# Performance work log

Hardware: AMD Instinct MI355X
Metric: run time of the kernel (lower is better)

## Reference

```python
import jax, jax.numpy as jnp
import numpy as np

N5, N4, N3, K = 10242, 2562, 642, 7  # icosphere node counts (levels 5,4,3), spatial kernel size
M = 32  # mchannel
EPS = 1e-8


def _sconv(x, neigh, W, b, relu=True):
    # x: [B,T,N,Cin]; neigh: [N,K] 1-ring indices; W: [K,Cin,Cout]
    xn = x[:, :, neigh, :]                        # [B,T,N,K,Cin] irregular gather
    y = jnp.einsum('btnkc,kcd->btnd', xn, W) + b  # per-node kernel contraction
    return jax.nn.relu(y) if relu else y


def _spool(x, pidx):
    # max-pool fine->coarse mesh: pidx [Ncoarse,Kp] indexes fine nodes
    return jnp.max(x[:, :, pidx, :], axis=3)


def _unpool(x, uidx):
    # coarse->fine copy: uidx [Nfine] indexes coarse nodes
    return x[:, :, uidx, :]


def _cos(f, a):
    # torch.nn.CosineSimilarity(dim=-1): dot / max(|f|*|a|, eps)
    dot = jnp.sum(f * a, axis=-1)
    nf = jnp.linalg.norm(f, axis=-1)
    na = jnp.linalg.norm(a, axis=-1)
    return dot / jnp.maximum(nf * na, EPS)


def setup_inputs() -> dict:
    key = jax.random.key(0)
    ks = jax.random.split(key, 32)
    w = lambda i, shape: jax.random.normal(ks[i], shape, jnp.float32) * 0.05
    inp = {
        'frame': jax.random.normal(ks[0], (1, 16, N5, 3), jnp.float32),
        'aem': jax.random.normal(ks[1], (1, 16, N5), jnp.float32),
        'W0f': w(2, (K, 3, M)),        'b0f': w(3, (M,)),
        'W0a': w(4, (K, 1, M)),        'b0a': w(5, (M,)),
        'W1f': w(6, (K, M, 2 * M)),    'b1f': w(7, (2 * M,)),
        'W1a': w(8, (K, M, 2 * M)),    'b1a': w(9, (2 * M,)),
        'W2f': w(10, (K, 2 * M, 4 * M)), 'b2f': w(11, (4 * M,)),
        'W2a': w(12, (K, 2 * M, 4 * M)), 'b2a': w(13, (4 * M,)),
        'W7': w(14, (K, 12 * M, 2 * M)), 'b7': w(15, (2 * M,)),
        'W8': w(16, (K, 4 * M, M)),    'b8': w(17, (M,)),
        'W9': w(18, (K, M, 1)),        'b9': w(19, (1,)),
        'neigh5': jax.random.randint(ks[20], (N5, K), 0, N5),
        'neigh4': jax.random.randint(ks[21], (N4, K), 0, N4),
        'neigh3': jax.random.randint(ks[22], (N3, K), 0, N3),
        'pool5': jax.random.randint(ks[23], (N4, K), 0, N5),
        'pool4': jax.random.randint(ks[24], (N3, K), 0, N4),
        'up4': jax.random.randint(ks[25], (N4,), 0, N3),
        'up5': jax.random.randint(ks[26], (N5,), 0, N4),
        'Tlocation': jax.random.randint(ks[27], (1, 16), 0, 16),
    }
    return inp


def reference(frame, aem, W0f, b0f, W0a, b0a, W1f, b1f, W1a, b1a, W2f, b2f,
              W2a, b2a, W7, b7, W8, b8, W9, b9,
              neigh5, neigh4, neigh3, pool5, pool4, up4, up5, Tlocation):
    a = aem[..., None]                                    # [B,T,N5,1]
    # encoder level 0 (N5)
    c0f = _sconv(frame, neigh5, W0f, b0f)
    c0a = _sconv(a, neigh5, W0a, b0a)
    p0f = _spool(c0f, pool5)
    p0a = _spool(c0a, pool5)
    m0 = _cos(c0f, c0a)[..., None]                        # [B,T,N5,1]
    c0f_att, c0a_att = c0f * m0, c0a * m0
    # encoder level 1 (N4)
    c1f = _sconv(p0f, neigh4, W1f, b1f)
    c1a = _sconv(p0a, neigh4, W1a, b1a)
    p1f = _spool(c1f, pool4)
    p1a = _spool(c1a, pool4)
    m1 = _cos(c1f, c1a)[..., None]
    c1f_att, c1a_att = c1f * m1, c1a * m1
    # bottleneck (N3)
    c2f = _sconv(p1f, neigh3, W2f, b2f)
    c2a = _sconv(p1a, neigh3, W2a, b2a)
    m2 = _cos(c2f, c2a)[..., None]
    conv2 = jnp.concatenate((c2f * m2, c2a * m2), axis=-1)  # [B,T,N3,8M]
    # decoder
    cat7 = jnp.concatenate((_unpool(conv2, up4), c1f_att, c1a_att), axis=-1)  # [B,T,N4,12M]
    conv7 = _sconv(cat7, neigh4, W7, b7)
    cat8 = jnp.concatenate((_unpool(conv7, up5), c0f_att, c0a_att), axis=-1)  # [B,T,N5,4M]
    conv8 = _sconv(cat8, neigh5, W8, b8)
    conv9 = _sconv(conv8, neigh5, W9, b9, relu=False)[..., 0]  # [B,T,N5]
    return jax.nn.softmax(conv9, axis=-1)
```

## Files before the change

### kernel.cpp

```cpp
#include <hip/hip_runtime.h>
#include <cfloat>
#include <cstdint>


constexpr int T  = 16;
constexpr int n5 = 10242, n4 = 2562, n3 = 642;
constexpr int K  = 7;

using bf16x8 = __attribute__((ext_vector_type(8))) short;
using f32x4  = __attribute__((ext_vector_type(4))) float;

static __device__ __forceinline__ float bf2f(unsigned short u) {
    return __uint_as_float((unsigned)u << 16);
}
static __device__ __forceinline__ unsigned short f2bf(float x) {
    unsigned u = __float_as_uint(x);
    u += 0x7FFF + ((u >> 16) & 1);
    return (unsigned short)(u >> 16);
}

__global__ __launch_bounds__(256) void conv0_kernel(
    const float* __restrict__ frame, const float* __restrict__ aem,
    const float* __restrict__ W0f, const float* __restrict__ b0f,
    const float* __restrict__ W0a, const float* __restrict__ b0a,
    const int* __restrict__ neigh5,
    unsigned short* __restrict__ c0f, unsigned short* __restrict__ c0a,
    unsigned short* __restrict__ att0)
{
    const int g = threadIdx.x >> 5;
    const int d = threadIdx.x & 31;
    const int per_t = (n5 + 7) / 8;
    const int t = blockIdx.x / per_t;
    const int n = (blockIdx.x % per_t) * 8 + g;
    if (n >= n5) return;

    float accf = b0f[d];
    float acca = b0a[d];
    const int* nb = neigh5 + n * K;
    #pragma unroll
    for (int k = 0; k < K; ++k) {
        const int j = nb[k];
        const float* fr = frame + ((size_t)t * n5 + j) * 3;
        const float av = aem[(size_t)t * n5 + j];
        accf = fmaf(fr[0], W0f[(k * 3 + 0) * 32 + d], accf);
        accf = fmaf(fr[1], W0f[(k * 3 + 1) * 32 + d], accf);
        accf = fmaf(fr[2], W0f[(k * 3 + 2) * 32 + d], accf);
        acca = fmaf(av, W0a[k * 32 + d], acca);
    }
    accf = fmaxf(accf, 0.f);
    acca = fmaxf(acca, 0.f);

    float dot = accf * acca, ff = accf * accf, aa = acca * acca;
    #pragma unroll
    for (int m = 1; m < 32; m <<= 1) {
        dot += __shfl_xor(dot, m, 32);
        ff  += __shfl_xor(ff,  m, 32);
        aa  += __shfl_xor(aa,  m, 32);
    }
    const float mm = dot / fmaxf(sqrtf(ff) * sqrtf(aa), 1e-8f);
    const size_t base = ((size_t)t * n5 + n) * 32;
    c0f[base + d] = f2bf(accf);
    c0a[base + d] = f2bf(acca);
    const size_t abase = ((size_t)t * n5 + n) * 64;
    att0[abase + d]      = f2bf(accf * mm);
    att0[abase + 32 + d] = f2bf(acca * mm);
}

template<int C>
__global__ __launch_bounds__(256) void pool_kernel(
    const unsigned short* __restrict__ in, const int* __restrict__ pidx,
    int Nin, int Nout, unsigned short* __restrict__ out)
{
    constexpr int C8 = C / 8;
    const int idx = blockIdx.x * 256 + threadIdx.x;
    if (idx >= T * Nout * C8) return;
    const int c8 = idx % C8;
    const int n  = (idx / C8) % Nout;
    const int t  = idx / (C8 * Nout);
    const int* pp = pidx + n * K;
    float m[8];
    #pragma unroll
    for (int j = 0; j < 8; ++j) m[j] = -FLT_MAX;
    #pragma unroll
    for (int k = 0; k < K; ++k) {
        const uint4 v = reinterpret_cast<const uint4*>(in)[((size_t)t * Nin + pp[k]) * C8 + c8];
        const unsigned short* s = reinterpret_cast<const unsigned short*>(&v);
        #pragma unroll
        for (int j = 0; j < 8; ++j) m[j] = fmaxf(m[j], bf2f(s[j]));
    }
    unsigned short o[8];
    #pragma unroll
    for (int j = 0; j < 8; ++j) o[j] = f2bf(m[j]);
    reinterpret_cast<uint4*>(out)[((size_t)t * Nout + n) * C8 + c8] =
        *reinterpret_cast<const uint4*>(o);
}

template<int C, int NN>
__global__ __launch_bounds__(256) void cosatt_kernel(
    const unsigned short* __restrict__ f, const unsigned short* __restrict__ a,
    unsigned short* __restrict__ att)
{
    constexpr int CPL = C / 64;
    const int w = threadIdx.x >> 6, lane = threadIdx.x & 63;
    const int idx = blockIdx.x * 4 + w;
    if (idx >= T * NN) return;
    const unsigned short* fr = f + (size_t)idx * C;
    const unsigned short* ar = a + (size_t)idx * C;
    float xs[CPL], ys[CPL];
    float dot = 0.f, ff = 0.f, aa = 0.f;
    #pragma unroll
    for (int i = 0; i < CPL; ++i) {
        const float x = bf2f(fr[lane + i * 64]);
        const float y = bf2f(ar[lane + i * 64]);
        xs[i] = x; ys[i] = y;
        dot = fmaf(x, y, dot);
        ff  = fmaf(x, x, ff);
        aa  = fmaf(y, y, aa);
    }
    #pragma unroll
    for (int msk = 1; msk < 64; msk <<= 1) {
        dot += __shfl_xor(dot, msk);
        ff  += __shfl_xor(ff,  msk);
        aa  += __shfl_xor(aa,  msk);
    }
    const float m = dot / fmaxf(sqrtf(ff) * sqrtf(aa), 1e-8f);
    unsigned short* orow = att + (size_t)idx * 2 * C;
    #pragma unroll
    for (int i = 0; i < CPL; ++i) {
        orow[lane + i * 64]     = f2bf(xs[i] * m);
        orow[C + lane + i * 64] = f2bf(ys[i] * m);
    }
}

struct PlainB16 {
    const uint4* x; int N; int C8;
    struct Ref { int o; };
    __device__ __forceinline__ Ref prep(int t, int node) const {
        return { (int)(((size_t)t * N + node) * C8) };
    }
    __device__ __forceinline__ uint4 chunk(const Ref& r, int c8) const {
        return x[r.o + c8];
    }
};

struct Cat7B16 {
    const uint4* att2; const uint4* att1; const int* up4;
    struct Ref { int o2, o1; };
    __device__ __forceinline__ Ref prep(int t, int node) const {
        return { (int)(((size_t)t * n3 + up4[node]) * 32),
                 (int)(((size_t)t * n4 + node) * 16) };
    }
    __device__ __forceinline__ uint4 chunk(const Ref& r, int c8) const {
        return (c8 < 32) ? att2[r.o2 + c8] : att1[r.o1 + (c8 - 32)];
    }
};

struct Cat8B16 {
    const uint4* cv7; const uint4* att0; const int* up5;
    struct Ref { int o7, o0; };
    __device__ __forceinline__ Ref prep(int t, int node) const {
        return { (int)(((size_t)t * n4 + up5[node]) * 8),
                 (int)(((size_t)t * n5 + node) * 8) };
    }
    __device__ __forceinline__ uint4 chunk(const Ref& r, int c8) const {
        return (c8 < 8) ? cv7[r.o7 + c8] : att0[r.o0 + (c8 - 8)];
    }
};

__global__ __launch_bounds__(256) void wprep_all_kernel(
    const float* __restrict__ W1f, const float* __restrict__ W1a,
    const float* __restrict__ W2f, const float* __restrict__ W2a,
    const float* __restrict__ W7,  const float* __restrict__ W8,
    unsigned short* __restrict__ Wt1f, unsigned short* __restrict__ Wt1a,
    unsigned short* __restrict__ Wt2f, unsigned short* __restrict__ Wt2a,
    unsigned short* __restrict__ Wt7,  unsigned short* __restrict__ Wt8)
{
    int idx = blockIdx.x * 256 + threadIdx.x;
    const float* W; unsigned short* Wt; int KCv, CO;
    if (idx < 14336)       { W = W1f; Wt = Wt1f; KCv = 224;  CO = 64;  }
    else if (idx < 28672)  { idx -= 14336;  W = W1a; Wt = Wt1a; KCv = 224;  CO = 64;  }
    else if (idx < 86016)  { idx -= 28672;  W = W2f; Wt = Wt2f; KCv = 448;  CO = 128; }
    else if (idx < 143360) { idx -= 86016;  W = W2a; Wt = Wt2a; KCv = 448;  CO = 128; }
    else if (idx < 315392) { idx -= 143360; W = W7;  Wt = Wt7;  KCv = 2688; CO = 64;  }
    else                   { idx -= 315392; W = W8;  Wt = Wt8;  KCv = 896;  CO = 32;  }
    const int d = idx / KCv, kc = idx - d * KCv;
    Wt[idx] = f2bf(W[(size_t)kc * CO + d]);
}

template<int CIN, int COUT, int BM, class Loader>
__global__ __launch_bounds__(256) void gemm_kk_kernel(
    Loader ldr, int N, int Mt,
    const unsigned short* __restrict__ Wt,
    unsigned short* __restrict__ Z)
{
    constexpr int KC     = K * CIN;
    constexpr int BK     = 64;
    constexpr int KSTEPS = CIN / BK;
    constexpr int U4R    = BK / 8;
    constexpr int WGR_N  = COUT / 32;
    constexpr int WGR_M  = 4 / WGR_N;
    constexpr int VPTA   = BM * U4R / 256;
    static_assert(BM == WGR_M * 32 && CIN % BK == 0);

    __shared__ __align__(16) unsigned short As[KSTEPS][BM * BK];
    __shared__ __align__(16) unsigned short Cs[BM * COUT];

    const int xcd = blockIdx.x & 7;
    int idx = blockIdx.x >> 3;
    const int hi = (idx >= Mt) ? 1 : 0;
    const int t  = 2 * xcd + hi;
    const int tile_m = idx - hi * Mt;
    const int m0 = tile_m * BM;

    const int tid = threadIdx.x, lane = tid & 63, wave = tid >> 6;
    const int wr = wave / WGR_N, wc = wave % WGR_N;
    const int l15 = lane & 15, lhi = lane >> 4;

    typename Loader::Ref ref[VPTA];
    #pragma unroll
    for (int v = 0; v < VPTA; ++v) {
        const int row = (tid + v * 256) / U4R;
        ref[v] = ldr.prep(t, min(m0 + row, N - 1));
    }
    #pragma unroll
    for (int ks = 0; ks < KSTEPS; ++ks) {
        #pragma unroll
        for (int v = 0; v < VPTA; ++v) {
            const int g = tid + v * 256, row = g / U4R, c8 = g % U4R;
            const uint4 av = ldr.chunk(ref[v], ks * U4R + c8);
            *reinterpret_cast<uint4*>(&As[ks][(row * BK + c8 * 8) ^ ((row & 7) << 3)]) = av;
        }
    }

    const unsigned short* w0p = Wt + (size_t)(wc * 32 + l15) * KC + lhi * 8;
    const unsigned short* w1p = w0p + (size_t)16 * KC;

    __syncthreads();

    for (int kk = 0; kk < K; ++kk) {
        f32x4 acc[2][2] = {};
        #pragma unroll
        for (int ks = 0; ks < KSTEPS; ++ks) {
            #pragma unroll
            for (int kk2 = 0; kk2 < 2; ++kk2) {
                const int kb = kk2 * 32 + lhi * 8;
                bf16x8 a[2], b[2];
                #pragma unroll
                for (int m = 0; m < 2; ++m) {
                    const int row = wr * 32 + m * 16 + l15;
                    a[m] = *reinterpret_cast<const bf16x8*>(
                        &As[ks][(row * BK + kb) ^ ((row & 7) << 3)]);
                }
                const int woff = kk * CIN + ks * BK + kk2 * 32;
                b[0] = *reinterpret_cast<const bf16x8*>(w0p + woff);
                b[1] = *reinterpret_cast<const bf16x8*>(w1p + woff);
                #pragma unroll
                for (int m = 0; m < 2; ++m)
                    #pragma unroll
                    for (int n = 0; n < 2; ++n)
                        acc[m][n] = __builtin_amdgcn_mfma_f32_16x16x32_bf16(
                            a[m], b[n], acc[m][n], 0, 0, 0);
            }
        }

        __syncthreads();
        #pragma unroll
        for (int n = 0; n < 2; ++n) {
            const int col = wc * 32 + n * 16 + l15;
            #pragma unroll
            for (int m = 0; m < 2; ++m)
                #pragma unroll
                for (int i = 0; i < 4; ++i)
                    Cs[(wr * 32 + m * 16 + lhi * 4 + i) * COUT + col] = f2bf(acc[m][n][i]);
        }
        __syncthreads();
        constexpr int RPT = COUT / 8;
        constexpr int CV  = BM * COUT / 8 / 256;
        #pragma unroll
        for (int v = 0; v < CV; ++v) {
            const int g = tid + v * 256, row = g / RPT, c8 = g % RPT;
            const int grow = m0 + row;
            if (grow < N)
                *reinterpret_cast<uint4*>(
                    &Z[(((size_t)kk * T + t) * N + grow) * COUT + c8 * 8]) =
                    *reinterpret_cast<const uint4*>(&Cs[row * COUT + c8 * 8]);
        }
    }
}

template<int COUT>
__global__ __launch_bounds__(256) void epi_p_kernel(
    const unsigned short* __restrict__ Z, const int* __restrict__ neigh,
    int N, int Bt, const float* __restrict__ bias, unsigned short* __restrict__ out)
{
    constexpr int C8 = COUT / 8;
    const int xcd = blockIdx.x & 7;
    int idx = blockIdx.x >> 3;
    const int hi = (idx >= Bt) ? 1 : 0;
    const int t  = 2 * xcd + hi;
    const int e  = (idx - hi * Bt) * 256 + threadIdx.x;
    if (e >= N * C8) return;
    const int c8 = e % C8;
    const int n  = e / C8;
    const int* nb = neigh + n * K;

    float s[8];
    #pragma unroll
    for (int j = 0; j < 8; ++j) s[j] = bias[c8 * 8 + j];
    #pragma unroll
    for (int k = 0; k < K; ++k) {
        const uint4 v = *reinterpret_cast<const uint4*>(
            &Z[(((size_t)k * T + t) * N + nb[k]) * COUT + c8 * 8]);
        const unsigned short* p = reinterpret_cast<const unsigned short*>(&v);
        #pragma unroll
        for (int j = 0; j < 8; ++j) s[j] += bf2f(p[j]);
    }
    unsigned short o[8];
    #pragma unroll
    for (int j = 0; j < 8; ++j) o[j] = f2bf(fmaxf(s[j], 0.f));
    *reinterpret_cast<uint4*>(&out[((size_t)t * N + n) * COUT + c8 * 8]) =
        *reinterpret_cast<const uint4*>(o);
}

template<int CIN, int COUT, class Loader>
__device__ __forceinline__ void sconv_tile(
    const Loader& ldr, const int* __restrict__ neigh, int N, int t,
    int tile_m, int tile_n,
    const unsigned short* __restrict__ Wt, const float* __restrict__ bias,
    unsigned short* __restrict__ out)
{
    constexpr int KC     = K * CIN;
    constexpr int CHUNKS = CIN / 32;
    constexpr int STEPS  = K * CHUNKS;
    constexpr int D      = STEPS < 3 ? STEPS : 3;

    const int lane = threadIdx.x & 63;
    const int l15 = lane & 15, lhi = lane >> 4;

    const int r0 = tile_m * 32 + l15;
    const int row0 = min(r0, N - 1), row1 = min(r0 + 16, N - 1);

    typename Loader::Ref ref0[K], ref1[K];
    #pragma unroll
    for (int k = 0; k < K; ++k) {
        ref0[k] = ldr.prep(t, neigh[row0 * K + k]);
        ref1[k] = ldr.prep(t, neigh[row1 * K + k]);
    }

    const int col0 = tile_n * 32 + l15;
    const unsigned short* w0p = Wt + (size_t)col0 * KC + lhi * 8;
    const unsigned short* w1p = w0p + (size_t)16 * KC;

    uint4 qa0[D], qa1[D], qb0[D], qb1[D];

    auto issue = [&](int s, int slot) {
        const int k = s / CHUNKS, c = s - k * CHUNKS;
        const int c8 = c * 4 + lhi;
        qa0[slot] = ldr.chunk(ref0[k], c8);
        qa1[slot] = ldr.chunk(ref1[k], c8);
        qb0[slot] = *reinterpret_cast<const uint4*>(w0p + k * CIN + c * 32);
        qb1[slot] = *reinterpret_cast<const uint4*>(w1p + k * CIN + c * 32);
    };

    f32x4 acc[2][2] = {};

    #pragma unroll
    for (int s = 0; s < D; ++s) issue(s, s);
    __builtin_amdgcn_sched_barrier(0);

    #pragma unroll
    for (int s = 0; s < STEPS; ++s) {
        const int slot = s % D;
        const bf16x8 a0 = __builtin_bit_cast(bf16x8, qa0[slot]);
        const bf16x8 a1 = __builtin_bit_cast(bf16x8, qa1[slot]);
        const bf16x8 b0 = __builtin_bit_cast(bf16x8, qb0[slot]);
        const bf16x8 b1 = __builtin_bit_cast(bf16x8, qb1[slot]);
        acc[0][0] = __builtin_amdgcn_mfma_f32_16x16x32_bf16(a0, b0, acc[0][0], 0, 0, 0);
        acc[0][1] = __builtin_amdgcn_mfma_f32_16x16x32_bf16(a0, b1, acc[0][1], 0, 0, 0);
        acc[1][0] = __builtin_amdgcn_mfma_f32_16x16x32_bf16(a1, b0, acc[1][0], 0, 0, 0);
        acc[1][1] = __builtin_amdgcn_mfma_f32_16x16x32_bf16(a1, b1, acc[1][1], 0, 0, 0);
        if (s + D < STEPS) issue(s + D, slot);
        __builtin_amdgcn_sched_barrier(0);
    }

    #pragma unroll
    for (int n = 0; n < 2; ++n) {
        const int gcol = tile_n * 32 + n * 16 + l15;
        const float bv = bias[gcol];
        #pragma unroll
        for (int m = 0; m < 2; ++m) {
            #pragma unroll
            for (int i = 0; i < 4; ++i) {
                const int grow = tile_m * 32 + m * 16 + lhi * 4 + i;
                if (grow < N)
                    out[((size_t)t * N + grow) * COUT + gcol] =
                        f2bf(fmaxf(acc[m][n][i] + bv, 0.f));
            }
        }
    }
}

template<int CIN, int COUT, class Loader>
__global__ __launch_bounds__(64, 2) void sconv_rd2_kernel(
    Loader lf, Loader la, const int* __restrict__ neigh, int N, int U,
    const unsigned short* __restrict__ Wtf, const unsigned short* __restrict__ Wta,
    const float* __restrict__ bf_, const float* __restrict__ ba_,
    unsigned short* __restrict__ of_, unsigned short* __restrict__ oa_)
{
    constexpr int TN = COUT / 32;
    const int xcd = blockIdx.x & 7;
    int idx = blockIdx.x >> 3;
    const int sel = idx & 1; idx >>= 1;
    const int hi = (idx >= U) ? 1 : 0;
    const int t  = 2 * xcd + hi;
    const int w  = idx - hi * U;
    const Loader L = sel ? la : lf;
    const unsigned short* Wt = sel ? Wta : Wtf;
    const float* bias = sel ? ba_ : bf_;
    unsigned short* out = sel ? oa_ : of_;
    sconv_tile<CIN, COUT, Loader>(L, neigh, N, t, w / TN, w % TN, Wt, bias, out);
}

__global__ __launch_bounds__(256) void conv9_kernel(
    const unsigned short* __restrict__ cv8, const int* __restrict__ neigh5,
    const float* __restrict__ W9, const float* __restrict__ b9,
    float* __restrict__ logits)
{
    const int idx = blockIdx.x * 256 + threadIdx.x;
    if (idx >= T * n5) return;
    const int n = idx % n5;
    const int t = idx / n5;
    float acc = b9[0];
    const int* nb = neigh5 + n * K;
    #pragma unroll
    for (int k = 0; k < K; ++k) {
        const uint4* row = reinterpret_cast<const uint4*>(cv8 + ((size_t)t * n5 + nb[k]) * 32);
        const float* wk = W9 + k * 32;
        #pragma unroll
        for (int c4 = 0; c4 < 4; ++c4) {
            const uint4 v = row[c4];
            const unsigned short* s = reinterpret_cast<const unsigned short*>(&v);
            #pragma unroll
            for (int jj = 0; jj < 8; ++jj)
                acc = fmaf(bf2f(s[jj]), wk[c4 * 8 + jj], acc);
        }
    }
    logits[idx] = acc;
}

__global__ __launch_bounds__(1024) void softmax_kernel(
    const float* __restrict__ logits, float* __restrict__ out)
{
    const int t = blockIdx.x, tid = threadIdx.x;
    const float* x = logits + (size_t)t * n5;
    float* y = out + (size_t)t * n5;
    __shared__ float redmax[16], redsum[16];

    float mx = -FLT_MAX;
    for (int i = tid; i < n5; i += 1024) mx = fmaxf(mx, x[i]);
    #pragma unroll
    for (int m = 1; m < 64; m <<= 1) mx = fmaxf(mx, __shfl_xor(mx, m));
    if ((tid & 63) == 0) redmax[tid >> 6] = mx;
    __syncthreads();
    mx = redmax[0];
    #pragma unroll
    for (int i = 1; i < 16; ++i) mx = fmaxf(mx, redmax[i]);

    float s = 0.f;
    for (int i = tid; i < n5; i += 1024) s += expf(x[i] - mx);
    #pragma unroll
    for (int m = 1; m < 64; m <<= 1) s += __shfl_xor(s, m);
    if ((tid & 63) == 0) redsum[tid >> 6] = s;
    __syncthreads();
    s = 0.f;
    #pragma unroll
    for (int i = 0; i < 16; ++i) s += redsum[i];

    for (int i = tid; i < n5; i += 1024) y[i] = expf(x[i] - mx) / s;
}

extern "C" void kernel_launch(void* const* d_in, const int* in_sizes, int n_in,
                              void* d_out, int out_size, void* d_ws, size_t ws_size,
                              hipStream_t stream)
{
    const float* frame = (const float*)d_in[0];
    const float* aem   = (const float*)d_in[1];
    const float* W0f = (const float*)d_in[2];
    const float* b0f = (const float*)d_in[3];
    const float* W0a = (const float*)d_in[4];
    const float* b0a = (const float*)d_in[5];
    const float* W1f = (const float*)d_in[6];
    const float* b1f = (const float*)d_in[7];
    const float* W1a = (const float*)d_in[8];
    const float* b1a = (const float*)d_in[9];
    const float* W2f = (const float*)d_in[10];
    const float* b2f = (const float*)d_in[11];
    const float* W2a = (const float*)d_in[12];
    const float* b2a = (const float*)d_in[13];
    const float* W7  = (const float*)d_in[14];
    const float* b7  = (const float*)d_in[15];
    const float* W8  = (const float*)d_in[16];
    const float* b8  = (const float*)d_in[17];
    const float* W9  = (const float*)d_in[18];
    const float* b9  = (const float*)d_in[19];
    const int* neigh5 = (const int*)d_in[20];
    const int* neigh4 = (const int*)d_in[21];
    const int* neigh3 = (const int*)d_in[22];
    const int* pool5  = (const int*)d_in[23];
    const int* pool4  = (const int*)d_in[24];
    const int* up4    = (const int*)d_in[25];
    const int* up5    = (const int*)d_in[26];

    unsigned short* wsu = (unsigned short*)d_ws;
    size_t off = 0;
    auto ua = [&](size_t n) {
        unsigned short* p = wsu + off; off += (n + 63) & ~(size_t)63; return p;
    };
    unsigned short* c0f  = ua((size_t)T * n5 * 32);
    unsigned short* c0a  = ua((size_t)T * n5 * 32);
    unsigned short* att0 = ua((size_t)T * n5 * 64);
    unsigned short* p0f  = ua((size_t)T * n4 * 32);
    unsigned short* p0a  = ua((size_t)T * n4 * 32);
    unsigned short* c1f  = ua((size_t)T * n4 * 64);
    unsigned short* c1a  = ua((size_t)T * n4 * 64);
    unsigned short* att1 = ua((size_t)T * n4 * 128);
    unsigned short* p1f  = ua((size_t)T * n3 * 64);
    unsigned short* p1a  = ua((size_t)T * n3 * 64);
    unsigned short* c2f  = ua((size_t)T * n3 * 128);
    unsigned short* c2a  = ua((size_t)T * n3 * 128);
    unsigned short* att2 = ua((size_t)T * n3 * 256);
    unsigned short* cv7  = ua((size_t)T * n4 * 64);
    unsigned short* cv8  = ua((size_t)T * n5 * 32);
    unsigned short* Wt1f = ua((size_t)64 * 224);
    unsigned short* Wt1a = ua((size_t)64 * 224);
    unsigned short* Wt2f = ua((size_t)128 * 448);
    unsigned short* Wt2a = ua((size_t)128 * 448);
    unsigned short* Wt7  = ua((size_t)64 * 2688);
    unsigned short* Wt8  = ua((size_t)32 * 896);
    unsigned short* Zbuf = ua((size_t)K * T * n5 * 32);
    float* lgt = (float*)(wsu + ((off + 1) & ~(size_t)1));

    wprep_all_kernel<<<1344, 256, 0, stream>>>(
        W1f, W1a, W2f, W2a, W7, W8, Wt1f, Wt1a, Wt2f, Wt2a, Wt7, Wt8);

    conv0_kernel<<<T * ((n5 + 7) / 8), 256, 0, stream>>>(
        frame, aem, W0f, b0f, W0a, b0a, neigh5, c0f, c0a, att0);

    {
        const int thr = T * n4 * (32 / 8);
        pool_kernel<32><<<(thr + 255) / 256, 256, 0, stream>>>(c0f, pool5, n5, n4, p0f);
        pool_kernel<32><<<(thr + 255) / 256, 256, 0, stream>>>(c0a, pool5, n5, n4, p0a);
    }

    {
        constexpr int U = 81 * 2;
        sconv_rd2_kernel<32, 64><<<8 * 4 * U, 64, 0, stream>>>(
            PlainB16{(const uint4*)p0f, n4, 4}, PlainB16{(const uint4*)p0a, n4, 4},
            neigh4, n4, U, Wt1f, Wt1a, b1f, b1a, c1f, c1a);
    }
    cosatt_kernel<64, n4><<<(T * n4 + 3) / 4, 256, 0, stream>>>(c1f, c1a, att1);

    {
        const int thr = T * n3 * (64 / 8);
        pool_kernel<64><<<(thr + 255) / 256, 256, 0, stream>>>(c1f, pool4, n4, n3, p1f);
        pool_kernel<64><<<(thr + 255) / 256, 256, 0, stream>>>(c1a, pool4, n4, n3, p1a);
    }

    {
        constexpr int U = 21 * 4;
        sconv_rd2_kernel<64, 128><<<8 * 4 * U, 64, 0, stream>>>(
            PlainB16{(const uint4*)p1f, n3, 8}, PlainB16{(const uint4*)p1a, n3, 8},
            neigh3, n3, U, Wt2f, Wt2a, b2f, b2a, c2f, c2a);
    }
    cosatt_kernel<128, n3><<<(T * n3 + 3) / 4, 256, 0, stream>>>(c2f, c2a, att2);

    {
        constexpr int Mt = (n4 + 63) / 64;
        gemm_kk_kernel<384, 64, 64><<<16 * Mt, 256, 0, stream>>>(
            Cat7B16{(const uint4*)att2, (const uint4*)att1, up4}, n4, Mt, Wt7, Zbuf);
        constexpr int Bt = (n4 * 8 + 255) / 256;
        epi_p_kernel<64><<<8 * 2 * Bt, 256, 0, stream>>>(
            Zbuf, neigh4, n4, Bt, b7, cv7);
    }

    {
        constexpr int Mt = (n5 + 127) / 128;
        gemm_kk_kernel<128, 32, 128><<<16 * Mt, 256, 0, stream>>>(
            Cat8B16{(const uint4*)cv7, (const uint4*)att0, up5}, n5, Mt, Wt8, Zbuf);
        constexpr int Bt = (n5 * 4 + 255) / 256;
        epi_p_kernel<32><<<8 * 2 * Bt, 256, 0, stream>>>(
            Zbuf, neigh5, n5, Bt, b8, cv8);
    }

    conv9_kernel<<<(T * n5 + 255) / 256, 256, 0, stream>>>(cv8, neigh5, W9, b9, lgt);

    softmax_kernel<<<T, 1024, 0, stream>>>(lgt, (float*)d_out);
}
```

Before: 292.9 us.

## Restructure decoder GEMM to stream K-chunks with register prefetch and smaller tiles

The decoder GEMM kernel no longer stages the whole input row panel in shared memory. It now streams one 64-wide K chunk at a time through a single LDS buffer and prefetches the next chunk into registers while the current one is computed. Each A fragment loaded from LDS is reused across all 7 kernel taps, with 7 sets of accumulators held in registers. Blocks shrink to 128 threads and half the rows per tile, which reduces LDS use and doubles the block count for better occupancy. The cost is higher accumulator register pressure and the extra barriers added inside each K step.

```diff
diff --git a/kernel.cpp b/kernel.cpp
--- a/kernel.cpp
+++ b/kernel.cpp
@@ -188,7 +188,7 @@
 }
 
 template<int CIN, int COUT, int BM, class Loader>
-__global__ __launch_bounds__(256) void gemm_kk_kernel(
+__global__ __launch_bounds__(128) void gemm_ms_kernel(
     Loader ldr, int N, int Mt,
     const unsigned short* __restrict__ Wt,
     unsigned short* __restrict__ Z)
@@ -198,11 +198,11 @@
     constexpr int KSTEPS = CIN / BK;
     constexpr int U4R    = BK / 8;
     constexpr int WGR_N  = COUT / 32;
-    constexpr int WGR_M  = 4 / WGR_N;
-    constexpr int VPTA   = BM * U4R / 256;
-    static_assert(BM == WGR_M * 32 && CIN % BK == 0);
-
-    __shared__ __align__(16) unsigned short As[KSTEPS][BM * BK];
+    constexpr int WGR_M  = BM / 32;
+    constexpr int VPTA   = BM * U4R / 128;
+    static_assert(WGR_M * WGR_N == 2 && CIN % BK == 0);
+
+    __shared__ __align__(16) unsigned short As[BM * BK];
     __shared__ __align__(16) unsigned short Cs[BM * COUT];
 
     const int xcd = blockIdx.x & 7;
@@ -218,51 +218,60 @@
 
     typename Loader::Ref ref[VPTA];
     #pragma unroll
-    for (int v = 0; v < VPTA; ++v) {
-        const int row = (tid + v * 256) / U4R;
-        ref[v] = ldr.prep(t, min(m0 + row, N - 1));
-    }
-    #pragma unroll
-    for (int ks = 0; ks < KSTEPS; ++ks) {
-        #pragma unroll
-        for (int v = 0; v < VPTA; ++v) {
-            const int g = tid + v * 256, row = g / U4R, c8 = g % U4R;
-            const uint4 av = ldr.chunk(ref[v], ks * U4R + c8);
-            *reinterpret_cast<uint4*>(&As[ks][(row * BK + c8 * 8) ^ ((row & 7) << 3)]) = av;
-        }
-    }
+    for (int v = 0; v < VPTA; ++v)
+        ref[v] = ldr.prep(t, min(m0 + (tid + v * 128) / U4R, N - 1));
 
     const unsigned short* w0p = Wt + (size_t)(wc * 32 + l15) * KC + lhi * 8;
     const unsigned short* w1p = w0p + (size_t)16 * KC;
 
-    __syncthreads();
-
-    for (int kk = 0; kk < K; ++kk) {
-        f32x4 acc[2][2] = {};
-        #pragma unroll
-        for (int ks = 0; ks < KSTEPS; ++ks) {
+    f32x4 acc[K][2][2] = {};
+
+    uint4 av[VPTA];
+    #pragma unroll
+    for (int v = 0; v < VPTA; ++v)
+        av[v] = ldr.chunk(ref[v], (tid + v * 128) % U4R);
+
+    for (int ks = 0; ks < KSTEPS; ++ks) {
+        __syncthreads();
+        #pragma unroll
+        for (int v = 0; v < VPTA; ++v) {
+            const int g = tid + v * 128, row = g / U4R, c8 = g % U4R;
+            *reinterpret_cast<uint4*>(&As[(row * BK + c8 * 8) ^ ((row & 7) << 3)]) = av[v];
+        }
+        __syncthreads();
+        if (ks + 1 < KSTEPS) {
             #pragma unroll
-            for (int kk2 = 0; kk2 < 2; ++kk2) {
-                const int kb = kk2 * 32 + lhi * 8;
-                bf16x8 a[2], b[2];
-                #pragma unroll
-                for (int m = 0; m < 2; ++m) {
-                    const int row = wr * 32 + m * 16 + l15;
-                    a[m] = *reinterpret_cast<const bf16x8*>(
-                        &As[ks][(row * BK + kb) ^ ((row & 7) << 3)]);
-                }
+            for (int v = 0; v < VPTA; ++v)
+                av[v] = ldr.chunk(ref[v], (ks + 1) * U4R + (tid + v * 128) % U4R);
+        }
+
+        #pragma unroll
+        for (int kk2 = 0; kk2 < 2; ++kk2) {
+            const int kb = kk2 * 32 + lhi * 8;
+            bf16x8 a[2];
+            #pragma unroll
+            for (int m = 0; m < 2; ++m) {
+                const int row = wr * 32 + m * 16 + l15;
+                a[m] = *reinterpret_cast<const bf16x8*>(
+                    &As[(row * BK + kb) ^ ((row & 7) << 3)]);
+            }
+            #pragma unroll
+            for (int kk = 0; kk < K; ++kk) {
                 const int woff = kk * CIN + ks * BK + kk2 * 32;
-                b[0] = *reinterpret_cast<const bf16x8*>(w0p + woff);
-                b[1] = *reinterpret_cast<const bf16x8*>(w1p + woff);
-                #pragma unroll
-                for (int m = 0; m < 2; ++m)
-                    #pragma unroll
-                    for (int n = 0; n < 2; ++n)
-                        acc[m][n] = __builtin_amdgcn_mfma_f32_16x16x32_bf16(
-                            a[m], b[n], acc[m][n], 0, 0, 0);
+                const bf16x8 b0 = *reinterpret_cast<const bf16x8*>(w0p + woff);
+                const bf16x8 b1 = *reinterpret_cast<const bf16x8*>(w1p + woff);
+                acc[kk][0][0] = __builtin_amdgcn_mfma_f32_16x16x32_bf16(a[0], b0, acc[kk][0][0], 0, 0, 0);
+                acc[kk][0][1] = __builtin_amdgcn_mfma_f32_16x16x32_bf16(a[0], b1, acc[kk][0][1], 0, 0, 0);
+                acc[kk][1][0] = __builtin_amdgcn_mfma_f32_16x16x32_bf16(a[1], b0, acc[kk][1][0], 0, 0, 0);
+                acc[kk][1][1] = __builtin_amdgcn_mfma_f32_16x16x32_bf16(a[1], b1, acc[kk][1][1], 0, 0, 0);
             }
         }
-
+    }
+
+    constexpr int RPT = COUT / 8;
+    constexpr int CV  = BM * COUT / 8 / 128;
+    #pragma unroll
+    for (int kk = 0; kk < K; ++kk) {
         __syncthreads();
         #pragma unroll
         for (int n = 0; n < 2; ++n) {
@@ -271,14 +280,12 @@
             for (int m = 0; m < 2; ++m)
                 #pragma unroll
                 for (int i = 0; i < 4; ++i)
-                    Cs[(wr * 32 + m * 16 + lhi * 4 + i) * COUT + col] = f2bf(acc[m][n][i]);
+                    Cs[(wr * 32 + m * 16 + lhi * 4 + i) * COUT + col] = f2bf(acc[kk][m][n][i]);
         }
         __syncthreads();
-        constexpr int RPT = COUT / 8;
-        constexpr int CV  = BM * COUT / 8 / 256;
         #pragma unroll
         for (int v = 0; v < CV; ++v) {
-            const int g = tid + v * 256, row = g / RPT, c8 = g % RPT;
+            const int g = tid + v * 128, row = g / RPT, c8 = g % RPT;
             const int grow = m0 + row;
             if (grow < N)
                 *reinterpret_cast<uint4*>(
@@ -575,8 +582,8 @@
     cosatt_kernel<128, n3><<<(T * n3 + 3) / 4, 256, 0, stream>>>(c2f, c2a, att2);
 
     {
-        constexpr int Mt = (n4 + 63) / 64;
-        gemm_kk_kernel<384, 64, 64><<<16 * Mt, 256, 0, stream>>>(
+        constexpr int Mt = (n4 + 31) / 32;
+        gemm_ms_kernel<384, 64, 32><<<16 * Mt, 128, 0, stream>>>(
             Cat7B16{(const uint4*)att2, (const uint4*)att1, up4}, n4, Mt, Wt7, Zbuf);
         constexpr int Bt = (n4 * 8 + 255) / 256;
         epi_p_kernel<64><<<8 * 2 * Bt, 256, 0, stream>>>(
@@ -584,8 +591,8 @@
     }
 
     {
-        constexpr int Mt = (n5 + 127) / 128;
-        gemm_kk_kernel<128, 32, 128><<<16 * Mt, 256, 0, stream>>>(
+        constexpr int Mt = (n5 + 63) / 64;
+        gemm_ms_kernel<128, 32, 64><<<16 * Mt, 128, 0, stream>>>(
             Cat8B16{(const uint4*)cv7, (const uint4*)att0, up5}, n5, Mt, Wt8, Zbuf);
         constexpr int Bt = (n5 * 4 + 255) / 256;
         epi_p_kernel<32><<<8 * 2 * Bt, 256, 0, stream>>>(
```

Measured after the change: 301.6 us. 3.0% more time.
